# Kernel tuning notes

Measured on AMD Instinct MI355X. Metric: run time of the kernel, lower is better.

Reference implementation:

```python
import jax, jax.numpy as jnp
import numpy as np

N_DIRS = 4
MAX_ITER = 5
GAMMA_MNODE = 2.0  # min_sum gamma_mnode from Params


def setup_inputs() -> dict:
    key = jax.random.key(0)
    B, H, W, L = 4, 256, 512, 21
    phi_i = jax.random.uniform(key, (B, H, W, L), dtype=jnp.float32) * 10.0  # unary costs
    eye = jnp.eye(L, dtype=jnp.float32)
    label_context = jnp.tile((1.0 - eye)[None], (N_DIRS, 1, 1))  # Potts init per __init__
    return {"phi_i": phi_i, "label_context": label_context}


def _sweep(unary, ctx):
    # unary: [S, B, R, L]; min-sum scanline recurrence along S (forward).
    # m_s(l') = min_l( unary_{s-1}(l) + m_{s-1}(l) + ctx(l, l') ), m_0 = 0.
    def step(m, u):
        tot = u + m  # [B, R, L]
        m_new = jnp.min(tot[..., :, None] + ctx, axis=-2)  # min over source label l
        m_new = m_new - jnp.min(m_new, axis=-1, keepdims=True)  # message normalization
        return m_new, m_new

    B, R, L = unary.shape[1:]
    init = jnp.zeros((B, R, L), unary.dtype)
    _, msgs = jax.lax.scan(step, init, unary[:-1])
    return jnp.concatenate([init[None], msgs], axis=0)  # [S, B, R, L]


def _dir_message(unary, ctx, d):
    # unary: [B, H, W, L]; d in {0: L->R, 1: R->L, 2: T->B, 3: B->T} (dir 0-3 of get_mode_params)
    if d == 0:
        u = jnp.transpose(unary, (2, 0, 1, 3))  # [W, B, H, L]
        m = _sweep(u, ctx)
        return jnp.transpose(m, (1, 2, 0, 3))
    if d == 1:
        u = jnp.transpose(unary[:, :, ::-1], (2, 0, 1, 3))
        m = _sweep(u, ctx)
        return jnp.transpose(m, (1, 2, 0, 3))[:, :, ::-1]
    if d == 2:
        u = jnp.transpose(unary, (1, 0, 2, 3))  # [H, B, W, L]
        m = _sweep(u, ctx)
        return jnp.transpose(m, (1, 0, 2, 3))
    u = jnp.transpose(unary[:, ::-1], (1, 0, 2, 3))
    m = _sweep(u, ctx)
    return jnp.transpose(m, (1, 0, 2, 3))[:, ::-1]


def reference(phi_i, label_context):
    # ISGMR-parallel min-sum directional message passing over a 2D grid.
    B, H, W, L = phi_i.shape
    msgs = jnp.zeros((N_DIRS, B, H, W, L), phi_i.dtype)
    for _ in range(MAX_ITER):
        total = phi_i + msgs.sum(0)  # aggregated cost
        msgs = jnp.stack(
            [_dir_message(total - msgs[d], label_context[d], d) for d in range(N_DIRS)], 0
        )
    # update_unary_belief (min_sum branch): phi_i * gamma_mnode + sum of messages
    unary_belief = phi_i * GAMMA_MNODE + msgs.sum(0)
    return unary_belief
```

## Files before the change

kernel.cpp:

```cpp
#include <hip/hip_runtime.h>

#define BB 4
#define HH 256
#define WW 512
#define LL 21
#define PIX (BB*HH*WW)
#define MSL 24
#define TSL 24
#define MFLD ((size_t)PIX*MSL)
#define PADV 1000.0f

#define CH 128
#define CHV 128
#define HA 32
#define FDV 16
#define HB 8

typedef float    fvec4 __attribute__((ext_vector_type(4)));
typedef _Float16 hvec4 __attribute__((ext_vector_type(4)));
typedef _Float16 hvec8 __attribute__((ext_vector_type(8)));
typedef unsigned uvec4 __attribute__((ext_vector_type(4)));

__device__ __forceinline__ fvec4 load4u(const float* p) {
    fvec4 v; __builtin_memcpy(&v, p, 16); return v;
}
__device__ __forceinline__ void store4u(float* p, fvec4 v) {
    __builtin_memcpy(p, &v, 16);
}

__global__ __launch_bounds__(256) void pad_kernel(
    const float* __restrict__ phi, _Float16* __restrict__ tot)
{
    int p = blockIdx.x * 256 + threadIdx.x;
    const float* pp = phi + (size_t)p * LL;
    float r[24];
    fvec4 u0 = load4u(pp + 0), u1 = load4u(pp + 4), u2 = load4u(pp + 8);
    fvec4 u3 = load4u(pp + 12), u4 = load4u(pp + 16);
    #pragma unroll
    for (int e = 0; e < 4; ++e) {
        r[e] = u0[e]; r[4+e] = u1[e]; r[8+e] = u2[e];
        r[12+e] = u3[e]; r[16+e] = u4[e];
    }
    r[20] = pp[20];
    r[21] = r[22] = r[23] = PADV;

    _Float16* op = tot + (size_t)p * TSL;
    #pragma unroll
    for (int c3 = 0; c3 < 3; ++c3) {
        hvec8 h;
        #pragma unroll
        for (int e = 0; e < 8; ++e) h[e] = (_Float16)r[8*c3 + e];
        *(hvec8*)(op + 8*c3) = h;
    }
}

__global__ __launch_bounds__(256) void ewise_kernel(
    const float* __restrict__ phi, const unsigned char* __restrict__ msgs,
    const float* __restrict__ scales,
    float* __restrict__ outf, _Float16* __restrict__ outh,
    float scale, int padded_out)
{
    int p = blockIdx.x * 256 + threadIdx.x;
    const float* pp = phi + (size_t)p * LL;

    float r[24];
    {
        fvec4 u0 = load4u(pp + 0), u1 = load4u(pp + 4), u2 = load4u(pp + 8);
        fvec4 u3 = load4u(pp + 12), u4 = load4u(pp + 16);
        #pragma unroll
        for (int e = 0; e < 4; ++e) {
            r[e]      = u0[e] * scale;
            r[4 + e]  = u1[e] * scale;
            r[8 + e]  = u2[e] * scale;
            r[12 + e] = u3[e] * scale;
            r[16 + e] = u4[e] * scale;
        }
        r[20] = pp[20] * scale;
        r[21] = r[22] = r[23] = 0.f;
    }

    fvec4 sc = load4u(scales);

    #pragma unroll
    for (int d = 0; d < 4; ++d) {
        const unsigned* mp =
            (const unsigned*)(msgs + (size_t)d * MFLD + (size_t)p * MSL);
        uint2 w0 = *(const uint2*)(mp + 0);
        uint2 w1 = *(const uint2*)(mp + 2);
        uint2 w2 = *(const uint2*)(mp + 4);
        unsigned w[6] = { w0.x, w0.y, w1.x, w1.y, w2.x, w2.y };
        float rs = sc[d] * (1.f / 255.f);
        #pragma unroll
        for (int j = 0; j < 21; ++j)
            r[j] += (float)((w[j >> 2] >> ((j & 3) * 8)) & 0xffu) * rs;
    }

    if (padded_out) {
        _Float16* op = outh + (size_t)p * TSL;
        r[21] = r[22] = r[23] = PADV;
        #pragma unroll
        for (int c3 = 0; c3 < 3; ++c3) {
            hvec8 h;
            #pragma unroll
            for (int e = 0; e < 8; ++e) h[e] = (_Float16)r[8*c3 + e];
            *(hvec8*)(op + 8*c3) = h;
        }
    } else {
        float* op = outf + (size_t)p * LL;
        store4u(op + 0,  *(const fvec4*)(r + 0));
        store4u(op + 4,  *(const fvec4*)(r + 4));
        store4u(op + 8,  *(const fvec4*)(r + 8));
        store4u(op + 12, *(const fvec4*)(r + 12));
        store4u(op + 16, *(const fvec4*)(r + 16));
        op[20] = r[20];
    }
}

__device__ __forceinline__ float min8(float x)
{
    int xi = __float_as_int(x); int y;
    y = __builtin_amdgcn_update_dpp(xi, xi, 0xB1, 0xf, 0xf, false);
    x = fminf(x, __int_as_float(y)); xi = __float_as_int(x);
    y = __builtin_amdgcn_update_dpp(xi, xi, 0x4E, 0xf, 0xf, false);
    x = fminf(x, __int_as_float(y)); xi = __float_as_int(x);
    y = __builtin_amdgcn_update_dpp(xi, xi, 0x141, 0xf, 0xf, false);
    x = fminf(x, __int_as_float(y));
    return x;
}
__device__ __forceinline__ float max8(float x)
{
    int xi = __float_as_int(x); int y;
    y = __builtin_amdgcn_update_dpp(xi, xi, 0xB1, 0xf, 0xf, false);
    x = fmaxf(x, __int_as_float(y)); xi = __float_as_int(x);
    y = __builtin_amdgcn_update_dpp(xi, xi, 0x4E, 0xf, 0xf, false);
    x = fmaxf(x, __int_as_float(y)); xi = __float_as_int(x);
    y = __builtin_amdgcn_update_dpp(xi, xi, 0x141, 0xf, 0xf, false);
    x = fmaxf(x, __int_as_float(y));
    return x;
}

template<bool FIRST>
__global__ __launch_bounds__(64) void sweep_kernel(
    const _Float16* __restrict__ tot, const float* __restrict__ ctx,
    unsigned char* __restrict__ msgs, float* __restrict__ scales)
{
    __shared__ __align__(16) unsigned char pool[11648];
    auto ltot = (unsigned char (*)[8][416])pool;
    auto lmsg = (unsigned char (*)[8][208])(pool + 6656);
    auto lout = (unsigned char (*)[208])(pool + 9984);
    float* shc  = (float*)pool;
    float* shrm = (float*)(pool + 1792);
    auto   sht  = (float (*)[24])(pool + 1920);

    const int lane = threadIdx.x;
    const int g = lane >> 3, k = lane & 7;
    const bool hz = (blockIdx.x < 1024);

    int d, chunk, r;
    int tstr, mstr;
    size_t pbase;
    if (hz) {
        int cl = blockIdx.x * 8 + g;
        chunk = cl >> 11;
        int line = cl & 2047;
        d = line >> 10;
        r = line & 1023;
        pbase = (size_t)r * WW;
        tstr = TSL; mstr = MSL;
        if (d == 1) { pbase += WW - 1; tstr = -tstr; mstr = -mstr; }
    } else {
        int cl = (blockIdx.x - 1024) * 8 + g;
        chunk = cl >> 12;
        int line = cl & 4095;
        d = 2 + (line >> 11);
        r = line & 2047;
        int bb = r >> 9, w = r & 511;
        pbase = (size_t)bb * HH * WW + w;
        tstr = WW * TSL; mstr = WW * MSL;
        if (d == 3) { pbase += (size_t)(HH - 1) * WW; tstr = -tstr; mstr = -mstr; }
    }
    const int CL = hz ? CH : CHV;
    const int ss = (chunk == 0) ? 0 : HA;
    const int sw = (chunk == 0) ? 0 : chunk * CL - HA;

    const float* ctxd = ctx + d * (LL * LL);
    const float  c    = ctxd[1];

    bool bad = (c < 0.f);
    float cmx = -1e30f, cmn = 1e30f;
    #pragma unroll
    for (int e = 0; e < 4; ++e) {
        int j = 4 * k + e;
        if (j < LL) {
            for (int l = 0; l < LL; ++l) {
                float v = ctxd[l * LL + j];
                float want = (l == j) ? 0.f : c;
                if (v != want) bad = true;
                cmx = fmaxf(cmx, v); cmn = fminf(cmn, v);
            }
        }
    }
    const bool potts = (__ballot(bad) == 0ull);
    const float R    = fmaxf(max8(cmx) - min8(cmn), 0.f);
    const float s255 = (R > 0.f) ? 255.f / R : 0.f;
    const float rs   = R * (1.f / 255.f);

    if (FIRST && lane == 0) scales[d] = R;

    const bool act = (k < 6);
    const int  koff = act ? 4 * k : 0;
    const bool dpos = ((d & 1) == 0);

    if (potts && hz) {
        const int r0 = r - g;
        const int sl = lane & 7;
        const int lg = lane >> 3;
        const char* tlineb = (const char*)tot
                             + (size_t)(r0 + sl) * ((size_t)WW * 48);
        unsigned char* mlineb = msgs + (size_t)d * MFLD
                              + (size_t)(r0 + sl) * ((size_t)WW * 24);

        const int NB  = (ss + CH) / HB;
        const int swb = ss / HB;

        uvec4 rt0, rt1, rt2;
        uvec4 rm0; uint2 rm1;

        auto wpix = [&](int b) {
            return dpos ? (sw + HB * b) : ((WW - HB) - sw - HB * b);
        };
        auto issue = [&](int b) {
            int wp = wpix(b);
            const char* tb = tlineb + (size_t)wp * 48;
            rt0 = *(const uvec4*)(tb + lg * 16);
            rt1 = *(const uvec4*)(tb + 128 + lg * 16);
            rt2 = *(const uvec4*)(tb + 256 + lg * 16);
            if (!FIRST) {
                const unsigned char* mq = mlineb + (size_t)wp * 24;
                rm0 = *(const uvec4*)(mq + lg * 16);
                rm1 = *(const uint2*)(mq + 128 + lg * 8);
            }
        };
        auto commit = [&](int b) {
            unsigned char* Lt = &ltot[b & 1][sl][0];
            *(uvec4*)(Lt + lg * 16)       = rt0;
            *(uvec4*)(Lt + 128 + lg * 16) = rt1;
            *(uvec4*)(Lt + 256 + lg * 16) = rt2;
            if (!FIRST) {
                unsigned char* Lm = &lmsg[b & 1][sl][0];
                *(uvec4*)(Lm + lg * 16)      = rm0;
                *(uint2*)(Lm + 128 + lg * 8) = rm1;
            }
        };
        auto flushb = [&](int b) {
            int wp = wpix(b);
            unsigned char* mq = mlineb + (size_t)wp * 24;
            const unsigned char* Lo = &lout[sl][0];
            uvec4 a = *(const uvec4*)(Lo + lg * 16);
            uint2 bq = *(const uint2*)(Lo + 128 + lg * 8);
            *(uvec4*)(mq + lg * 16)      = a;
            *(uint2*)(mq + 128 + lg * 8) = bq;
        };

        float mn0 = 0.f, mn1 = 0.f, mn2 = 0.f, mn3 = 0.f, tminp = 0.f;

        issue(0); commit(0);
        issue(1);
        for (int b = 0; b < NB; ++b) {
            const bool st = (b >= swb);

            hvec4 th8[HB]; unsigned wd8[HB];
            {
                const unsigned char* Lt = &ltot[b & 1][g][0];
                const unsigned char* Lm = &lmsg[b & 1][g][0];
                #pragma unroll
                for (int i = 0; i < HB; ++i) {
                    int p = dpos ? i : HB - 1 - i;
                    th8[i] = *(const hvec4*)(Lt + p * 48 + 2 * koff);
                    wd8[i] = FIRST ? 0u : *(const unsigned*)(Lm + p * 24 + koff);
                }
            }
            if (b + 1 < NB) commit(b + 1);
            if (b + 2 < NB) issue(b + 2);

            #pragma unroll
            for (int i = 0; i < HB; ++i) {
                int p = dpos ? i : HB - 1 - i;
                if (st && act) {
                    float off = fmaf(-tminp, s255, 0.5f);
                    unsigned q0 = (unsigned)fmaf(mn0, s255, off);
                    unsigned q1 = (unsigned)fmaf(mn1, s255, off);
                    unsigned q2 = (unsigned)fmaf(mn2, s255, off);
                    unsigned q3 = (unsigned)fmaf(mn3, s255, off);
                    *(unsigned*)(&lout[g][0] + p * 24 + 4 * k) =
                        q0 | (q1 << 8) | (q2 << 16) | (q3 << 24);
                }
                hvec4 th = th8[i]; unsigned wd = wd8[i];
                float T0, T1, T2, T3;
                if (FIRST) {
                    T0 = (float)th[0] + mn0; T1 = (float)th[1] + mn1;
                    T2 = (float)th[2] + mn2; T3 = (float)th[3] + mn3;
                } else {
                    T0 = fmaf(-rs, (float)( wd        & 0xffu), (float)th[0]) + mn0;
                    T1 = fmaf(-rs, (float)((wd >>  8) & 0xffu), (float)th[1]) + mn1;
                    T2 = fmaf(-rs, (float)((wd >> 16) & 0xffu), (float)th[2]) + mn2;
                    T3 = fmaf(-rs, (float)( wd >> 24        ), (float)th[3]) + mn3;
                }
                float lm = fminf(fminf(T0, T1), fminf(T2, T3));
                lm = min8(lm);
                float Q = lm + c;
                mn0 = fminf(T0, Q); mn1 = fminf(T1, Q);
                mn2 = fminf(T2, Q); mn3 = fminf(T3, Q);
                tminp = lm;
            }
            if (st) flushb(b);
        }
    } else if (potts) {
        const _Float16* tp = tot + pbase * TSL + koff + (ptrdiff_t)sw * tstr;
        unsigned char*  mb = msgs + (size_t)d * MFLD + pbase * MSL + koff
                                  + (ptrdiff_t)sw * mstr;

        hvec4 tf[FDV]; unsigned mfq[FDV];
        #pragma unroll
        for (int i = 0; i < FDV; ++i) {
            tf[i] = *(const hvec4*)(tp + (ptrdiff_t)i * tstr);
            mfq[i] = FIRST ? 0u : *(const unsigned*)(mb + (ptrdiff_t)i * mstr);
        }
        const _Float16* tld = tp + (ptrdiff_t)FDV * tstr;
        const unsigned char* mld = mb + (ptrdiff_t)FDV * mstr;
        unsigned char* mst = mb;

        float mn0 = 0.f, mn1 = 0.f, mn2 = 0.f, mn3 = 0.f, tminp = 0.f;

        auto vstep = [&](hvec4 th, unsigned wd, bool st) {
            if (st && act) {
                float off = fmaf(-tminp, s255, 0.5f);
                unsigned q0 = (unsigned)fmaf(mn0, s255, off);
                unsigned q1 = (unsigned)fmaf(mn1, s255, off);
                unsigned q2 = (unsigned)fmaf(mn2, s255, off);
                unsigned q3 = (unsigned)fmaf(mn3, s255, off);
                *(unsigned*)mst = q0 | (q1 << 8) | (q2 << 16) | (q3 << 24);
            }
            mst += mstr;
            float T0, T1, T2, T3;
            if (FIRST) {
                T0 = (float)th[0] + mn0; T1 = (float)th[1] + mn1;
                T2 = (float)th[2] + mn2; T3 = (float)th[3] + mn3;
            } else {
                T0 = fmaf(-rs, (float)( wd        & 0xffu), (float)th[0]) + mn0;
                T1 = fmaf(-rs, (float)((wd >>  8) & 0xffu), (float)th[1]) + mn1;
                T2 = fmaf(-rs, (float)((wd >> 16) & 0xffu), (float)th[2]) + mn2;
                T3 = fmaf(-rs, (float)( wd >> 24        ), (float)th[3]) + mn3;
            }
            float lm = fminf(fminf(T0, T1), fminf(T2, T3));
            lm = min8(lm);
            float Q = lm + c;
            mn0 = fminf(T0, Q); mn1 = fminf(T1, Q);
            mn2 = fminf(T2, Q); mn3 = fminf(T3, Q);
            tminp = lm;
        };

        const int nout = (ss + CHV - FDV) / FDV;
        for (int j = 0; j < nout; ++j) {
            const bool st = (FDV * j >= ss);
            #pragma unroll
            for (int i = 0; i < FDV; ++i) {
                hvec4 th = tf[i]; unsigned wd = mfq[i];
                tf[i] = *(const hvec4*)tld;
                if (!FIRST) mfq[i] = *(const unsigned*)mld;
                tld += tstr; mld += mstr;
                vstep(th, wd, st);
            }
        }
        #pragma unroll
        for (int i = 0; i < FDV; ++i) vstep(tf[i], mfq[i], true);
    } else {
        for (int i = lane; i < LL * LL; i += 64) shc[i] = ctxd[i];
        __syncthreads();
        if (lane < LL) {
            float mn = shc[lane * LL];
            for (int j = 1; j < LL; ++j) mn = fminf(mn, shc[lane * LL + j]);
            shrm[lane] = mn;
        }
        __syncthreads();

        const bool okA = (k < 6);
        const bool okB = (k < 5);
        const _Float16* tp = tot + pbase * TSL + koff + (ptrdiff_t)sw * tstr;
        const unsigned char* mld = msgs + (size_t)d * MFLD + pbase * MSL + koff
                                        + (ptrdiff_t)sw * mstr;
        unsigned char* mst = (unsigned char*)mld;

        float m0 = 0.f, m1 = 0.f, m2 = 0.f, m3 = 0.f;
        const int j0 = (4 * k     < LL) ? 4 * k     : LL - 1;
        const int j1 = (4 * k + 1 < LL) ? 4 * k + 1 : LL - 1;
        const int j2 = (4 * k + 2 < LL) ? 4 * k + 2 : LL - 1;
        const int j3 = (4 * k + 3 < LL) ? 4 * k + 3 : LL - 1;

        const int total = ss + CL;
        for (int t = 0; t < total; ++t) {
            const bool st = (t >= ss);
            if (st && act) {
                unsigned q0 = (unsigned)fminf(fmaf(m0, s255, 0.5f), 255.f);
                unsigned q1 = (unsigned)fminf(fmaf(m1, s255, 0.5f), 255.f);
                unsigned q2 = (unsigned)fminf(fmaf(m2, s255, 0.5f), 255.f);
                unsigned q3 = (unsigned)fminf(fmaf(m3, s255, 0.5f), 255.f);
                *(unsigned*)mst = q0 | (q1 << 8) | (q2 << 16) | (q3 << 24);
            }
            hvec4 th = *(const hvec4*)(tp + (ptrdiff_t)t * tstr);
            unsigned wd = FIRST ? 0u
                : *(const unsigned*)(mld + (ptrdiff_t)t * mstr);
            mst += mstr;
            float t0, t1, t2, t3;
            if (FIRST) {
                t0 = (float)th[0] + m0; t1 = (float)th[1] + m1;
                t2 = (float)th[2] + m2; t3 = (float)th[3] + m3;
            } else {
                t0 = fmaf(-rs, (float)( wd        & 0xffu), (float)th[0]) + m0;
                t1 = fmaf(-rs, (float)((wd >>  8) & 0xffu), (float)th[1]) + m1;
                t2 = fmaf(-rs, (float)((wd >> 16) & 0xffu), (float)th[2]) + m2;
                t3 = fmaf(-rs, (float)( wd >> 24        ), (float)th[3]) + m3;
            }
            __syncthreads();
            if (okA) sht[g][4 * k] = t0;
            if (okB) {
                sht[g][4 * k + 1] = t1;
                sht[g][4 * k + 2] = t2;
                sht[g][4 * k + 3] = t3;
            }
            __syncthreads();
            float mnA = 1e30f, mnB = 1e30f, mnC = 1e30f, mnD = 1e30f;
            float gm  = 1e30f;
            for (int l = 0; l < LL; ++l) {
                float tl = sht[g][l];
                mnA = fminf(mnA, tl + shc[l * LL + j0]);
                mnB = fminf(mnB, tl + shc[l * LL + j1]);
                mnC = fminf(mnC, tl + shc[l * LL + j2]);
                mnD = fminf(mnD, tl + shc[l * LL + j3]);
                gm  = fminf(gm,  tl + shrm[l]);
            }
            m0 = mnA - gm; m1 = mnB - gm; m2 = mnC - gm; m3 = mnD - gm;
        }
    }
}

extern "C" void kernel_launch(void* const* d_in, const int* in_sizes, int n_in,
                              void* d_out, int out_size, void* d_ws, size_t ws_size,
                              hipStream_t stream)
{
    (void)in_sizes; (void)n_in; (void)out_size; (void)ws_size;

    const float* phi = (const float*)d_in[0];
    const float* ctx = (const float*)d_in[1];
    float* out = (float*)d_out;

    unsigned char* msgs = (unsigned char*)d_ws;
    _Float16* totp = (_Float16*)((char*)d_ws + 4 * MFLD);
    float* scales  = (float*)((char*)totp + (size_t)PIX * TSL * sizeof(_Float16));

    const int EW_BLOCKS = PIX / 256;
    const int SW_BLOCKS = 1024 + 1024;

    pad_kernel<<<EW_BLOCKS, 256, 0, stream>>>(phi, totp);

    sweep_kernel<true><<<SW_BLOCKS, 64, 0, stream>>>(totp, ctx, msgs, scales);

    for (int it = 1; it < 5; ++it) {
        ewise_kernel<<<EW_BLOCKS, 256, 0, stream>>>(phi, msgs, scales,
                                                    nullptr, totp, 1.0f, 1);
        sweep_kernel<false><<<SW_BLOCKS, 64, 0, stream>>>(totp, ctx, msgs, scales);
    }

    ewise_kernel<<<EW_BLOCKS, 256, 0, stream>>>(phi, msgs, scales,
                                                out, nullptr, 2.0f, 0);
}
```

Baseline: 395.5 us.

## Ping-pong message buffers and halve sweep chunk length to double block count

```diff
diff --git a/kernel.cpp b/kernel.cpp
--- a/kernel.cpp
+++ b/kernel.cpp
@@ -10,8 +10,6 @@
 #define MFLD ((size_t)PIX*MSL)
 #define PADV 1000.0f
 
-#define CH 128
-#define CHV 128
 #define HA 32
 #define FDV 16
 #define HB 8
@@ -142,7 +140,8 @@
 template<bool FIRST>
 __global__ __launch_bounds__(64) void sweep_kernel(
     const _Float16* __restrict__ tot, const float* __restrict__ ctx,
-    unsigned char* __restrict__ msgs, float* __restrict__ scales)
+    const unsigned char* __restrict__ msrc, unsigned char* __restrict__ mdst,
+    float* __restrict__ scales, int fine)
 {
     __shared__ __align__(16) unsigned char pool[11648];
     auto ltot = (unsigned char (*)[8][416])pool;
@@ -154,7 +153,9 @@
 
     const int lane = threadIdx.x;
     const int g = lane >> 3, k = lane & 7;
-    const bool hz = (blockIdx.x < 1024);
+    const int hzB = fine ? 2048 : 1024;
+    const bool hz = ((int)blockIdx.x < hzB);
+    const int CL = fine ? 64 : 128;
 
     int d, chunk, r;
     int tstr, mstr;
@@ -169,7 +170,7 @@
         tstr = TSL; mstr = MSL;
         if (d == 1) { pbase += WW - 1; tstr = -tstr; mstr = -mstr; }
     } else {
-        int cl = (blockIdx.x - 1024) * 8 + g;
+        int cl = (blockIdx.x - hzB) * 8 + g;
         chunk = cl >> 12;
         int line = cl & 4095;
         d = 2 + (line >> 11);
@@ -179,7 +180,6 @@
         tstr = WW * TSL; mstr = WW * MSL;
         if (d == 3) { pbase += (size_t)(HH - 1) * WW; tstr = -tstr; mstr = -mstr; }
     }
-    const int CL = hz ? CH : CHV;
     const int ss = (chunk == 0) ? 0 : HA;
     const int sw = (chunk == 0) ? 0 : chunk * CL - HA;
 
@@ -217,10 +217,12 @@
         const int lg = lane >> 3;
         const char* tlineb = (const char*)tot
                              + (size_t)(r0 + sl) * ((size_t)WW * 48);
-        unsigned char* mlineb = msgs + (size_t)d * MFLD
+        const unsigned char* mlinesrc = msrc + (size_t)d * MFLD
                               + (size_t)(r0 + sl) * ((size_t)WW * 24);
-
-        const int NB  = (ss + CH) / HB;
+        unsigned char* mlinedst = mdst + (size_t)d * MFLD
+                              + (size_t)(r0 + sl) * ((size_t)WW * 24);
+
+        const int NB  = (ss + CL) / HB;
         const int swb = ss / HB;
 
         uvec4 rt0, rt1, rt2;
@@ -236,7 +238,7 @@
             rt1 = *(const uvec4*)(tb + 128 + lg * 16);
             rt2 = *(const uvec4*)(tb + 256 + lg * 16);
             if (!FIRST) {
-                const unsigned char* mq = mlineb + (size_t)wp * 24;
+                const unsigned char* mq = mlinesrc + (size_t)wp * 24;
                 rm0 = *(const uvec4*)(mq + lg * 16);
                 rm1 = *(const uint2*)(mq + 128 + lg * 8);
             }
@@ -254,7 +256,7 @@
         };
         auto flushb = [&](int b) {
             int wp = wpix(b);
-            unsigned char* mq = mlineb + (size_t)wp * 24;
+            unsigned char* mq = mlinedst + (size_t)wp * 24;
             const unsigned char* Lo = &lout[sl][0];
             uvec4 a = *(const uvec4*)(Lo + lg * 16);
             uint2 bq = *(const uint2*)(Lo + 128 + lg * 8);
@@ -317,18 +319,20 @@
         }
     } else if (potts) {
         const _Float16* tp = tot + pbase * TSL + koff + (ptrdiff_t)sw * tstr;
-        unsigned char*  mb = msgs + (size_t)d * MFLD + pbase * MSL + koff
+        const unsigned char* mbs = msrc + (size_t)d * MFLD + pbase * MSL + koff
+                                  + (ptrdiff_t)sw * mstr;
+        unsigned char* mbd = mdst + (size_t)d * MFLD + pbase * MSL + koff
                                   + (ptrdiff_t)sw * mstr;
 
         hvec4 tf[FDV]; unsigned mfq[FDV];
         #pragma unroll
         for (int i = 0; i < FDV; ++i) {
             tf[i] = *(const hvec4*)(tp + (ptrdiff_t)i * tstr);
-            mfq[i] = FIRST ? 0u : *(const unsigned*)(mb + (ptrdiff_t)i * mstr);
+            mfq[i] = FIRST ? 0u : *(const unsigned*)(mbs + (ptrdiff_t)i * mstr);
         }
         const _Float16* tld = tp + (ptrdiff_t)FDV * tstr;
-        const unsigned char* mld = mb + (ptrdiff_t)FDV * mstr;
-        unsigned char* mst = mb;
+        const unsigned char* mld = mbs + (ptrdiff_t)FDV * mstr;
+        unsigned char* mst = mbd;
 
         float mn0 = 0.f, mn1 = 0.f, mn2 = 0.f, mn3 = 0.f, tminp = 0.f;
 
@@ -360,7 +364,7 @@
             tminp = lm;
         };
 
-        const int nout = (ss + CHV - FDV) / FDV;
+        const int nout = (ss + CL - FDV) / FDV;
         for (int j = 0; j < nout; ++j) {
             const bool st = (FDV * j >= ss);
             #pragma unroll
@@ -387,9 +391,10 @@
         const bool okA = (k < 6);
         const bool okB = (k < 5);
         const _Float16* tp = tot + pbase * TSL + koff + (ptrdiff_t)sw * tstr;
-        const unsigned char* mld = msgs + (size_t)d * MFLD + pbase * MSL + koff
+        const unsigned char* mld = msrc + (size_t)d * MFLD + pbase * MSL + koff
                                         + (ptrdiff_t)sw * mstr;
-        unsigned char* mst = (unsigned char*)mld;
+        unsigned char* mst = mdst + (size_t)d * MFLD + pbase * MSL + koff
+                                  + (ptrdiff_t)sw * mstr;
 
         float m0 = 0.f, m1 = 0.f, m2 = 0.f, m3 = 0.f;
         const int j0 = (4 * k     < LL) ? 4 * k     : LL - 1;
@@ -448,29 +453,39 @@
                               void* d_out, int out_size, void* d_ws, size_t ws_size,
                               hipStream_t stream)
 {
-    (void)in_sizes; (void)n_in; (void)out_size; (void)ws_size;
+    (void)in_sizes; (void)n_in; (void)out_size;
 
     const float* phi = (const float*)d_in[0];
     const float* ctx = (const float*)d_in[1];
     float* out = (float*)d_out;
 
-    unsigned char* msgs = (unsigned char*)d_ws;
-    _Float16* totp = (_Float16*)((char*)d_ws + 4 * MFLD);
-    float* scales  = (float*)((char*)totp + (size_t)PIX * TSL * sizeof(_Float16));
+    const size_t totB = (size_t)PIX * TSL * sizeof(_Float16);
+    const size_t needPP = 8 * MFLD + totB + 1024;
+    const bool pp = (ws_size >= needPP);
+
+    unsigned char* A = (unsigned char*)d_ws;
+    unsigned char* B = pp ? A + 4 * MFLD : A;
+    _Float16* totp = (_Float16*)(A + (pp ? 8 : 4) * MFLD);
+    float* scales  = (float*)((char*)totp + totB);
 
     const int EW_BLOCKS = PIX / 256;
-    const int SW_BLOCKS = 1024 + 1024;
+    const int SW_BLOCKS = pp ? 4096 : 2048;
+    const int fine = pp ? 1 : 0;
 
     pad_kernel<<<EW_BLOCKS, 256, 0, stream>>>(phi, totp);
 
-    sweep_kernel<true><<<SW_BLOCKS, 64, 0, stream>>>(totp, ctx, msgs, scales);
-
+    sweep_kernel<true><<<SW_BLOCKS, 64, 0, stream>>>(totp, ctx, A, A,
+                                                     scales, fine);
+    unsigned char* cur = A;
     for (int it = 1; it < 5; ++it) {
-        ewise_kernel<<<EW_BLOCKS, 256, 0, stream>>>(phi, msgs, scales,
+        ewise_kernel<<<EW_BLOCKS, 256, 0, stream>>>(phi, cur, scales,
                                                     nullptr, totp, 1.0f, 1);
-        sweep_kernel<false><<<SW_BLOCKS, 64, 0, stream>>>(totp, ctx, msgs, scales);
-    }
-
-    ewise_kernel<<<EW_BLOCKS, 256, 0, stream>>>(phi, msgs, scales,
+        unsigned char* nxt = pp ? (cur == A ? B : A) : A;
+        sweep_kernel<false><<<SW_BLOCKS, 64, 0, stream>>>(totp, ctx, cur, nxt,
+                                                          scales, fine);
+        cur = nxt;
+    }
+
+    ewise_kernel<<<EW_BLOCKS, 256, 0, stream>>>(phi, cur, scales,
                                                 out, nullptr, 2.0f, 0);
 }
```

Measured after the change: 432.3 us. 9.3% more time.
